# Performance work log

Measured on AMD Instinct MI355X. Metric: run time of the kernel, lower is better.

Reference implementation:

```python
import jax, jax.numpy as jnp
import numpy as np

C = 256      # in_channels
NH = 4       # n_heads
NG = 32      # GroupNorm num_groups
EPS = 1e-5   # torch GroupNorm default eps


def _conv1x1(x, w, b):
    # 1x1 conv == per-pixel channel matmul. x: (B,C,H,W), w: (O,C), b: (O,)
    return jnp.einsum('oc,bchw->bohw', w, x) + b[None, :, None, None]


def _groupnorm(x, gamma, beta):
    b, c, h, w = x.shape
    xg = x.reshape(b, NG, c // NG, h, w)
    mu = xg.mean(axis=(2, 3, 4), keepdims=True)
    var = xg.var(axis=(2, 3, 4), keepdims=True)
    xn = ((xg - mu) * jax.lax.rsqrt(var + EPS)).reshape(b, c, h, w)
    return xn * gamma[None, :, None, None] + beta[None, :, None, None]


def setup_inputs() -> dict:
    key = jax.random.key(0)
    ks = jax.random.split(key, 5)
    B, H, W = 2, 64, 64
    s = 1.0 / np.sqrt(C).astype(np.float32)
    return {
        'x': jax.random.normal(ks[0], (B, C, H, W), jnp.float32),
        'gamma': jnp.ones((C,), jnp.float32),
        'beta': jnp.zeros((C,), jnp.float32),
        'wq': jax.random.normal(ks[1], (C, C), jnp.float32) * s,
        'bq': jnp.zeros((C,), jnp.float32),
        'wk': jax.random.normal(ks[2], (C, C), jnp.float32) * s,
        'bk': jnp.zeros((C,), jnp.float32),
        'wv': jax.random.normal(ks[3], (C, C), jnp.float32) * s,
        'bv': jnp.zeros((C,), jnp.float32),
        'wp': jax.random.normal(ks[4], (C, C), jnp.float32) * s,
        'bp': jnp.zeros((C,), jnp.float32),
    }


def reference(x, gamma, beta, wq, bq, wk, bk, wv, bv, wp, bp):
    b, c, h, w = x.shape
    c_ = c // NH  # head dim
    hn = _groupnorm(x, gamma, beta)
    # NOTE: original splits channels as (head_dim, n_heads) with head_dim leading
    q = _conv1x1(hn, wq, bq).reshape(b, c_, NH, h * w)
    k = _conv1x1(hn, wk, bk).reshape(b, c_, NH, h * w)
    v = _conv1x1(hn, wv, bv).reshape(b, c_, NH, h * w)
    scores = jnp.einsum('bcnq,bcnk->bqkn', q, k) * (c_ ** -0.5)  # (B,S,S,NH)
    attn = jax.nn.softmax(scores, axis=2)  # softmax over key axis
    out = jnp.einsum('bcnd,bqdn->bcnq', v, attn).reshape(b, c, h, w)
    return x + _conv1x1(out, wp, bp)
```

## Files before the change

kernel.cpp:

```cpp
#include <hip/hip_runtime.h>

#define CH 256
#define NHEAD 4
#define HD 64
#define SP 4096
#define NB 2
#define QSCALE 0.1803368801111204f

typedef __attribute__((ext_vector_type(8))) short bf16x8;
typedef __attribute__((ext_vector_type(4))) float f32x4;
typedef unsigned int u32;
typedef unsigned short u16;

__device__ inline u16 b16(float f) {
    u32 u = __float_as_uint(f);
    return (u16)((u + 0x8000u) >> 16);
}
__device__ inline u32 bpack(float lo, float hi) {
    u32 ul = __float_as_uint(lo), uh = __float_as_uint(hi);
    return ((uh + 0x8000u) & 0xffff0000u) | ((ul + 0x8000u) >> 16);
}
__device__ inline float fexp2(float x) { return __builtin_amdgcn_exp2f(x); }

__global__ __launch_bounds__(256) void prep_kernel(
    const float* __restrict__ x, float2* __restrict__ part,
    const float* __restrict__ wq, const float* __restrict__ wk,
    const float* __restrict__ wv, const float* __restrict__ wp,
    u16* __restrict__ wqb, u16* __restrict__ wkb,
    u16* __restrict__ wvb, u16* __restrict__ wpb)
{
    int tid = threadIdx.x;
    if (blockIdx.x < 256) {
        int bgq = blockIdx.x;
        int bg = bgq >> 2, qtr = bgq & 3;
        const float4* xp = (const float4*)(x + (size_t)bg * 8 * SP) + qtr * 2048;
        float s = 0.f, ss = 0.f;
        for (int i = tid; i < 2048; i += 256) {
            float4 u = xp[i];
            s  += (u.x + u.y) + (u.z + u.w);
            ss += (u.x * u.x + u.y * u.y) + (u.z * u.z + u.w * u.w);
        }
#pragma unroll
        for (int off = 32; off > 0; off >>= 1) {
            s  += __shfl_down(s, off);
            ss += __shfl_down(ss, off);
        }
        __shared__ float ws_s[4], ws_q[4];
        int w = tid >> 6;
        if ((tid & 63) == 0) { ws_s[w] = s; ws_q[w] = ss; }
        __syncthreads();
        if (tid == 0)
            part[bgq] = make_float2(ws_s[0] + ws_s[1] + ws_s[2] + ws_s[3],
                                    ws_q[0] + ws_q[1] + ws_q[2] + ws_q[3]);
    } else {
        int idx = (blockIdx.x - 256) * 256 + tid;
        int m = idx >> 16, i = idx & 65535;
        if (m == 0)      wqb[i] = b16(wq[i] * QSCALE);
        else if (m == 1) wkb[i] = b16(wk[i]);
        else if (m == 2) wvb[i] = b16(wv[i]);
        else {
            int c = i >> 8, col = i & 255;
            int n = col & 3, d = col >> 2;
            wpb[c * 256 + n * 64 + d] = b16(wp[i]);
        }
    }
}

__global__ __launch_bounds__(256) void qkv_gemm_kernel(
    const float* __restrict__ x, const float2* __restrict__ part,
    const float* __restrict__ gamma, const float* __restrict__ beta,
    const u16* __restrict__ wqb, const u16* __restrict__ wkb,
    const u16* __restrict__ wvb,
    const float* __restrict__ bq, const float* __restrict__ bk,
    const float* __restrict__ bv,
    u16* __restrict__ qt, u16* __restrict__ ktp, u16* __restrict__ vtp)
{
    int zz = blockIdx.y;
    int b = zz / 3, p = zz % 3;
    const u16* W = (p == 0) ? wqb : (p == 1) ? wkb : wvb;
    const float* bias = (p == 0) ? bq : (p == 1) ? bk : bv;
    float bs = (p == 0) ? QSCALE : 1.f;
    int s0 = blockIdx.x * 32;
    int tid = threadIdx.x, w = tid >> 6, lane = tid & 63;
    int t = lane >> 4, ln = lane & 15;

    __shared__ u16 SB[10240];
    __shared__ float As[256], Bs[256];

    {
        int c = tid, bg = b * 32 + (c >> 3);
        float s = 0.f, ss = 0.f;
#pragma unroll
        for (int q = 0; q < 4; q++) { float2 pp = part[bg * 4 + q]; s += pp.x; ss += pp.y; }
        float mu = s * (1.f / 32768.f);
        float var = ss * (1.f / 32768.f) - mu * mu;
        float rs = rsqrtf(var + 1e-5f);
        float ga = gamma[c];
        As[c] = rs * ga;
        Bs[c] = beta[c] - mu * rs * ga;
    }
    __syncthreads();

    {
        int c2 = (tid >> 3) * 2;
        int sseg = (tid & 7) * 4;
#pragma unroll
        for (int it = 0; it < 4; it++) {
            int c = it * 64 + c2;
            float4 v0 = *(const float4*)&x[((size_t)b * CH + c) * SP + s0 + sseg];
            float4 v1 = *(const float4*)&x[((size_t)b * CH + c + 1) * SP + s0 + sseg];
            float a0 = As[c], b0 = Bs[c], a1 = As[c + 1], b1 = Bs[c + 1];
            float e0[4] = {fmaf(a0, v0.x, b0), fmaf(a0, v0.y, b0),
                           fmaf(a0, v0.z, b0), fmaf(a0, v0.w, b0)};
            float e1[4] = {fmaf(a1, v1.x, b1), fmaf(a1, v1.y, b1),
                           fmaf(a1, v1.z, b1), fmaf(a1, v1.w, b1)};
#pragma unroll
            for (int j = 0; j < 4; j++)
                *(u32*)&SB[(sseg + j) * 264 + c] = bpack(e0[j], e1[j]);
        }
    }
    __syncthreads();

    f32x4 acc[4][2];
#pragma unroll
    for (int og = 0; og < 4; og++)
#pragma unroll
        for (int sg = 0; sg < 2; sg++)
            acc[og][sg] = (f32x4){0.f, 0.f, 0.f, 0.f};

#pragma unroll
    for (int ks = 0; ks < 8; ks++) {
        bf16x8 af[4], bfv[2];
#pragma unroll
        for (int og = 0; og < 4; og++)
            af[og] = *(const bf16x8*)&W[(size_t)(w * 64 + og * 16 + ln) * CH + ks * 32 + t * 8];
#pragma unroll
        for (int sg = 0; sg < 2; sg++)
            bfv[sg] = *(const bf16x8*)&SB[(sg * 16 + ln) * 264 + ks * 32 + t * 8];
#pragma unroll
        for (int og = 0; og < 4; og++)
#pragma unroll
            for (int sg = 0; sg < 2; sg++)
                acc[og][sg] = __builtin_amdgcn_mfma_f32_16x16x32_bf16(
                    af[og], bfv[sg], acc[og][sg], 0, 0, 0);
    }
    __syncthreads();

    if (p < 2) {
#pragma unroll
        for (int og = 0; og < 4; og++)
#pragma unroll
            for (int sg = 0; sg < 2; sg++)
#pragma unroll
                for (int r = 0; r < 4; r++) {
                    int o = w * 64 + og * 16 + 4 * t + r;
                    SB[(r * 32 + sg * 16 + ln) * 72 + (w * 16 + og * 4 + t)] =
                        b16(acc[og][sg][r] + bias[o] * bs);
                }
        __syncthreads();
        if (p == 0) {
#pragma unroll
            for (int it = 0; it < 4; it++) {
                int f = it * 256 + tid;
                int o8 = f & 7, sl = (f >> 3) & 31, n = f >> 8;
                *(uint4*)&qt[((size_t)(b * 4 + n) * SP + s0 + sl) * HD + o8 * 8] =
                    *(const uint4*)&SB[(n * 32 + sl) * 72 + o8 * 8];
            }
        } else {
#pragma unroll
            for (int it = 0; it < 4; it++) {
                int f = it * 256 + tid;
                int o8 = f & 7, sl = (f >> 3) & 31, n = f >> 8;
                int key = s0 + sl;
                int g = ((key >> 4) & 3) * 2 + (o8 >> 2);
                int lp = (key & 15) + 16 * (o8 & 3);
                *(uint4*)&ktp[(size_t)(b * 4 + n) * SP * HD +
                              (size_t)(key >> 6) * 4096 + g * 512 + lp * 8] =
                    *(const uint4*)&SB[(n * 32 + sl) * 72 + o8 * 8];
            }
        }
    } else {
#pragma unroll
        for (int og = 0; og < 4; og++)
#pragma unroll
            for (int sg = 0; sg < 2; sg++)
#pragma unroll
                for (int r = 0; r < 4; r++) {
                    int o = w * 64 + og * 16 + 4 * t + r;
                    SB[(r * 64 + w * 16 + og * 4 + t) * 40 + sg * 16 + ln] =
                        b16(acc[og][sg][r] + bias[o]);
                }
        __syncthreads();
#pragma unroll
        for (int it = 0; it < 4; it++) {
            int f = it * 256 + tid;
            int so8 = f & 3, d = (f >> 2) & 63, n = f >> 8;
            int key = s0 + so8 * 8;
            int g = ((d >> 4) & 3) * 2 + ((key >> 5) & 1);
            int lp = (d & 15) + 16 * ((key >> 3) & 3);
            *(uint4*)&vtp[(size_t)(b * 4 + n) * SP * HD +
                          (size_t)(key >> 6) * 4096 + g * 512 + lp * 8] =
                *(const uint4*)&SB[(n * 64 + d) * 40 + so8 * 8];
        }
    }
}

template <int NT>
__global__ __launch_bounds__(256, 3) void attn_kernel(
    const u16* __restrict__ qtb, const u16* __restrict__ ktp,
    const u16* __restrict__ vtp, u16* __restrict__ opart,
    float* __restrict__ lpart)
{
    int bx = blockIdx.x;
    int z = bx & 7, qt_i = (bx >> 3) & 31, sp = bx >> 8;
    int sq0 = qt_i * 128;
    int tile0 = sp * NT;
    const u16* qz = qtb + (size_t)z * SP * HD;
    const u16* kz = ktp + (size_t)z * SP * HD;
    const u16* vz = vtp + (size_t)z * SP * HD;

    int tid = threadIdx.x, w = tid >> 6, l = tid & 63;
    int t = l >> 4, ln = l & 15;

    __shared__ __align__(16) u32 Pb[4][2][512];

    bf16x8 qf[2][2];
#pragma unroll
    for (int qg = 0; qg < 2; qg++)
#pragma unroll
        for (int ds = 0; ds < 2; ds++)
            qf[qg][ds] = *(const bf16x8*)&qz[
                (size_t)(sq0 + w * 32 + qg * 16 + ln) * HD + ds * 32 + t * 8];

    bf16x8 kf[8], vf[8];
#pragma unroll
    for (int g = 0; g < 8; g++)
        kf[g] = *(const bf16x8*)&kz[(size_t)tile0 * 4096 + g * 512 + l * 8];

    float lsum[2] = {0.f, 0.f};
    f32x4 oacc[2][4];
#pragma unroll
    for (int qg = 0; qg < 2; qg++)
#pragma unroll
        for (int dg = 0; dg < 4; dg++)
            oacc[qg][dg] = (f32x4){0.f, 0.f, 0.f, 0.f};

    const f32x4 z4 = {0.f, 0.f, 0.f, 0.f};
    f32x4 sa[2][4];

    auto ep = [&](int qg) {
#pragma unroll
        for (int kg = 0; kg < 4; kg++) {
            float e0 = fexp2(sa[qg][kg][0]);
            float e1 = fexp2(sa[qg][kg][1]);
            float e2 = fexp2(sa[qg][kg][2]);
            float e3 = fexp2(sa[qg][kg][3]);
            lsum[qg] += (e0 + e1) + (e2 + e3);
            u32 p0 = __builtin_amdgcn_perm(__float_as_uint(e1), __float_as_uint(e0), 0x07060302u);
            u32 p1 = __builtin_amdgcn_perm(__float_as_uint(e3), __float_as_uint(e2), 0x07060302u);
            int Lt = ln + 16 * (2 * (kg & 1) + (t >> 1));
            int ksg = kg >> 1;
            *(uint2*)&Pb[w][qg][(ksg * 64 + Lt) * 4 + 2 * (t & 1)] =
                make_uint2(p0, p1);
        }
    };

#pragma unroll
    for (int kti = 0; kti < NT; kti++) {
        size_t tb = (size_t)(tile0 + kti) * 4096;

#pragma unroll
        for (int g = 0; g < 8; g++)
            vf[g] = *(const bf16x8*)&vz[tb + g * 512 + l * 8];

#pragma unroll
        for (int kg = 0; kg < 4; kg++)
#pragma unroll
            for (int qg = 0; qg < 2; qg++)
                sa[qg][kg] = __builtin_amdgcn_mfma_f32_16x16x32_bf16(
                    kf[kg * 2 + 0], qf[qg][0], z4, 0, 0, 0);
#pragma unroll
        for (int kg = 0; kg < 4; kg++)
#pragma unroll
            for (int qg = 0; qg < 2; qg++)
                sa[qg][kg] = __builtin_amdgcn_mfma_f32_16x16x32_bf16(
                    kf[kg * 2 + 1], qf[qg][1], sa[qg][kg], 0, 0, 0);

        if (kti < NT - 1) {
            size_t nb = tb + 4096;
#pragma unroll
            for (int g = 0; g < 8; g++)
                kf[g] = *(const bf16x8*)&kz[nb + g * 512 + l * 8];
        }

        ep(0);
#pragma unroll
        for (int qg = 0; qg < 2; qg++) {
            if (qg == 0) ep(1);
            bf16x8 pf[2];
#pragma unroll
            for (int ksg = 0; ksg < 2; ksg++)
                pf[ksg] = *(const bf16x8*)&Pb[w][qg][(ksg * 64 + l) * 4];
#pragma unroll
            for (int ksg = 0; ksg < 2; ksg++)
#pragma unroll
                for (int dg = 0; dg < 4; dg++)
                    oacc[qg][dg] = __builtin_amdgcn_mfma_f32_16x16x32_bf16(
                        pf[ksg], vf[dg * 2 + ksg], oacc[qg][dg], 0, 0, 0);
        }
    }

#pragma unroll
    for (int qg = 0; qg < 2; qg++) {
        lsum[qg] += __shfl_xor(lsum[qg], 16);
        lsum[qg] += __shfl_xor(lsum[qg], 32);
    }

    size_t obase = (size_t)(sp * 8 + z) * SP;
    u16* po = (u16*)&Pb[w][0][0];
#pragma unroll
    for (int qg = 0; qg < 2; qg++)
#pragma unroll
        for (int dg = 0; dg < 4; dg++)
#pragma unroll
            for (int r = 0; r < 4; r++)
                po[(qg * 16 + 4 * t + r) * 64 + dg * 16 + ln] = b16(oacc[qg][dg][r]);
#pragma unroll
    for (int i = 0; i < 4; i++) {
        int f = i * 512 + l * 8;
        int qloc = f >> 6, d0 = f & 63;
        uint4 v = *(const uint4*)&po[f];
        *(uint4*)&opart[(obase + sq0 + w * 32 + qloc) * HD + d0] = v;
    }
    if (t == 0)
#pragma unroll
        for (int qg = 0; qg < 2; qg++)
            lpart[obase + sq0 + w * 32 + qg * 16 + ln] = lsum[qg];
}

template <int NSPLIT>
__global__ __launch_bounds__(256) void proj_gemm_kernel(
    const u16* __restrict__ opart, const float* __restrict__ lpart,
    const u16* __restrict__ wpb, const float* __restrict__ bp,
    const float* __restrict__ x, float* __restrict__ out)
{
    int b = blockIdx.y;
    int s0 = blockIdx.x * 16;
    int tid = threadIdx.x, w = tid >> 6, lane = tid & 63;
    int t = lane >> 4, ln = lane & 15;

    __shared__ u16 BsL[16 * 264];

#pragma unroll
    for (int it = 0; it < 2; it++) {
        int f = it * 256 + tid;
        int oct = f & 31, s = f >> 5;
        int n = oct >> 3, d0 = (oct & 7) * 8;
        float lsumv = 0.f;
        float accv[8] = {0.f,0.f,0.f,0.f,0.f,0.f,0.f,0.f};
#pragma unroll
        for (int sp = 0; sp < NSPLIT; sp++) {
            size_t base = (size_t)(sp * 8 + b * 4 + n) * SP + s0 + s;
            lsumv += lpart[base];
            uint4 o4 = *(const uint4*)&opart[base * HD + d0];
            u32 ov[4] = {o4.x, o4.y, o4.z, o4.w};
#pragma unroll
            for (int i = 0; i < 4; i++) {
                accv[2 * i + 0] += __uint_as_float(ov[i] << 16);
                accv[2 * i + 1] += __uint_as_float(ov[i] & 0xffff0000u);
            }
        }
        float inv = 1.f / lsumv;
        u32 res[4];
#pragma unroll
        for (int i = 0; i < 4; i++)
            res[i] = (bpack(accv[2 * i + 0] * inv, accv[2 * i + 1] * inv));
        *(uint4*)&BsL[s * 264 + oct * 8] = make_uint4(res[0], res[1], res[2], res[3]);
    }
    __syncthreads();

    f32x4 acc[4];
#pragma unroll
    for (int og = 0; og < 4; og++)
        acc[og] = (f32x4){0.f, 0.f, 0.f, 0.f};

#pragma unroll
    for (int ks = 0; ks < 8; ks++) {
        bf16x8 af[4];
#pragma unroll
        for (int og = 0; og < 4; og++)
            af[og] = *(const bf16x8*)&wpb[(size_t)(w * 64 + og * 16 + ln) * CH + ks * 32 + t * 8];
        bf16x8 bfv = *(const bf16x8*)&BsL[ln * 264 + ks * 32 + t * 8];
#pragma unroll
        for (int og = 0; og < 4; og++)
            acc[og] = __builtin_amdgcn_mfma_f32_16x16x32_bf16(
                af[og], bfv, acc[og], 0, 0, 0);
    }

#pragma unroll
    for (int og = 0; og < 4; og++)
#pragma unroll
        for (int r = 0; r < 4; r++) {
            int c = w * 64 + og * 16 + 4 * t + r;
            size_t idx = ((size_t)b * CH + c) * SP + s0 + ln;
            out[idx] = acc[og][r] + bp[c] + x[idx];
        }
}

extern "C" void kernel_launch(void* const* d_in, const int* in_sizes, int n_in,
                              void* d_out, int out_size, void* d_ws, size_t ws_size,
                              hipStream_t stream)
{
    const float* x     = (const float*)d_in[0];
    const float* gamma = (const float*)d_in[1];
    const float* beta  = (const float*)d_in[2];
    const float* wq = (const float*)d_in[3]; const float* bq = (const float*)d_in[4];
    const float* wk = (const float*)d_in[5]; const float* bk = (const float*)d_in[6];
    const float* wv = (const float*)d_in[7]; const float* bv = (const float*)d_in[8];
    const float* wp = (const float*)d_in[9]; const float* bp = (const float*)d_in[10];
    float* out = (float*)d_out;

    const size_t TEN = (size_t)8 * SP * HD;
    const size_t NEED8 = 4096 + 524288 + 3 * TEN * 2 + 8 * TEN * 2 + 8 * 8 * SP * 4;
    int nsplit = (ws_size >= NEED8) ? 8 : 4;

    char* wsb = (char*)d_ws;
    float2* part = (float2*)wsb;
    u16* wqb = (u16*)(wsb + 4096);
    u16* wkb = wqb + 65536;
    u16* wvb = wkb + 65536;
    u16* wpb = wvb + 65536;
    u16* qt  = wpb + 65536;
    u16* ktp = qt + TEN;
    u16* vtp = ktp + TEN;
    u16* opart = vtp + TEN;
    float* lpart = (float*)(opart + (size_t)nsplit * TEN);

    prep_kernel<<<dim3(1280), dim3(256), 0, stream>>>(
        x, part, wq, wk, wv, wp, wqb, wkb, wvb, wpb);
    qkv_gemm_kernel<<<dim3(128, 6), dim3(256), 0, stream>>>(
        x, part, gamma, beta, wqb, wkb, wvb, bq, bk, bv, qt, ktp, vtp);
    if (nsplit == 8) {
        attn_kernel<8><<<dim3(2048), dim3(256), 0, stream>>>(
            qt, ktp, vtp, opart, lpart);
        proj_gemm_kernel<8><<<dim3(256, 2), dim3(256), 0, stream>>>(
            opart, lpart, wpb, bp, x, out);
    } else {
        attn_kernel<16><<<dim3(1024), dim3(256), 0, stream>>>(
            qt, ktp, vtp, opart, lpart);
        proj_gemm_kernel<4><<<dim3(256, 2), dim3(256), 0, stream>>>(
            opart, lpart, wpb, bp, x, out);
    }
}
```

Before: 155.0 us.

## Fuse four kernels into one persistent cooperative kernel with grid syncs

Merges the prep, QKV GEMM, attention and projection kernels into one persistent cooperative kernel. Blocks loop over work units for each phase, and grid.sync separates the phases. The aim is to remove the launch overhead and tail gaps between kernels. In exchange it caps occupancy through launch bounds and the occupancy query, adds grid-wide barrier costs, and may lose the higher parallelism of the attention launch.

```diff
diff --git a/kernel.cpp b/kernel.cpp
--- a/kernel.cpp
+++ b/kernel.cpp
@@ -1,10 +1,12 @@
 #include <hip/hip_runtime.h>
+#include <hip/hip_cooperative_groups.h>
+
+namespace cg = cooperative_groups;
 
 #define CH 256
 #define NHEAD 4
 #define HD 64
 #define SP 4096
-#define NB 2
 #define QSCALE 0.1803368801111204f
 
 typedef __attribute__((ext_vector_type(8))) short bf16x8;
@@ -22,389 +24,398 @@
 }
 __device__ inline float fexp2(float x) { return __builtin_amdgcn_exp2f(x); }
 
-__global__ __launch_bounds__(256) void prep_kernel(
+template <int NT>
+__global__ __launch_bounds__(256, 3) void fused_kernel(
     const float* __restrict__ x, float2* __restrict__ part,
+    const float* __restrict__ gamma, const float* __restrict__ beta,
     const float* __restrict__ wq, const float* __restrict__ wk,
     const float* __restrict__ wv, const float* __restrict__ wp,
+    const float* __restrict__ bq, const float* __restrict__ bk,
+    const float* __restrict__ bv, const float* __restrict__ bp,
     u16* __restrict__ wqb, u16* __restrict__ wkb,
-    u16* __restrict__ wvb, u16* __restrict__ wpb)
+    u16* __restrict__ wvb, u16* __restrict__ wpb,
+    u16* __restrict__ qt, u16* __restrict__ ktp, u16* __restrict__ vtp,
+    u16* __restrict__ opart, float* __restrict__ lpart,
+    float* __restrict__ out)
 {
+    constexpr int NSPLIT = 64 / NT;
+    cg::grid_group grid = cg::this_grid();
+    __shared__ __align__(16) char smem[22784];
+
     int tid = threadIdx.x;
-    if (blockIdx.x < 256) {
-        int bgq = blockIdx.x;
-        int bg = bgq >> 2, qtr = bgq & 3;
-        const float4* xp = (const float4*)(x + (size_t)bg * 8 * SP) + qtr * 2048;
-        float s = 0.f, ss = 0.f;
-        for (int i = tid; i < 2048; i += 256) {
-            float4 u = xp[i];
-            s  += (u.x + u.y) + (u.z + u.w);
-            ss += (u.x * u.x + u.y * u.y) + (u.z * u.z + u.w * u.w);
-        }
-#pragma unroll
-        for (int off = 32; off > 0; off >>= 1) {
-            s  += __shfl_down(s, off);
-            ss += __shfl_down(ss, off);
-        }
-        __shared__ float ws_s[4], ws_q[4];
-        int w = tid >> 6;
-        if ((tid & 63) == 0) { ws_s[w] = s; ws_q[w] = ss; }
-        __syncthreads();
-        if (tid == 0)
-            part[bgq] = make_float2(ws_s[0] + ws_s[1] + ws_s[2] + ws_s[3],
-                                    ws_q[0] + ws_q[1] + ws_q[2] + ws_q[3]);
-    } else {
-        int idx = (blockIdx.x - 256) * 256 + tid;
-        int m = idx >> 16, i = idx & 65535;
-        if (m == 0)      wqb[i] = b16(wq[i] * QSCALE);
-        else if (m == 1) wkb[i] = b16(wk[i]);
-        else if (m == 2) wvb[i] = b16(wv[i]);
-        else {
-            int c = i >> 8, col = i & 255;
-            int n = col & 3, d = col >> 2;
-            wpb[c * 256 + n * 64 + d] = b16(wp[i]);
+    int nb = gridDim.x, bid = blockIdx.x;
+    int w = tid >> 6, lane = tid & 63;
+    int t = lane >> 4, ln = lane & 15;
+
+    for (int u = bid; u < 1280; u += nb) {
+        if (u < 256) {
+            int bg = u >> 2, qtr = u & 3;
+            const float4* xp = (const float4*)(x + (size_t)bg * 8 * SP) + qtr * 2048;
+            float s = 0.f, ss = 0.f;
+            for (int i = tid; i < 2048; i += 256) {
+                float4 v = xp[i];
+                s  += (v.x + v.y) + (v.z + v.w);
+                ss += (v.x * v.x + v.y * v.y) + (v.z * v.z + v.w * v.w);
+            }
+#pragma unroll
+            for (int off = 32; off > 0; off >>= 1) {
+                s  += __shfl_down(s, off);
+                ss += __shfl_down(ss, off);
+            }
+            float* ws_s = (float*)smem;
+            float* ws_q = (float*)smem + 4;
+            __syncthreads();
+            if (lane == 0) { ws_s[w] = s; ws_q[w] = ss; }
+            __syncthreads();
+            if (tid == 0)
+                part[u] = make_float2(ws_s[0] + ws_s[1] + ws_s[2] + ws_s[3],
+                                      ws_q[0] + ws_q[1] + ws_q[2] + ws_q[3]);
+        } else {
+            int idx = (u - 256) * 256 + tid;
+            int m = idx >> 16, i = idx & 65535;
+            if (m == 0)      wqb[i] = b16(wq[i] * QSCALE);
+            else if (m == 1) wkb[i] = b16(wk[i]);
+            else if (m == 2) wvb[i] = b16(wv[i]);
+            else {
+                int c = i >> 8, col = i & 255;
+                int n = col & 3, d = col >> 2;
+                wpb[c * 256 + n * 64 + d] = b16(wp[i]);
+            }
         }
     }
-}
-
-__global__ __launch_bounds__(256) void qkv_gemm_kernel(
-    const float* __restrict__ x, const float2* __restrict__ part,
-    const float* __restrict__ gamma, const float* __restrict__ beta,
-    const u16* __restrict__ wqb, const u16* __restrict__ wkb,
-    const u16* __restrict__ wvb,
-    const float* __restrict__ bq, const float* __restrict__ bk,
-    const float* __restrict__ bv,
-    u16* __restrict__ qt, u16* __restrict__ ktp, u16* __restrict__ vtp)
-{
-    int zz = blockIdx.y;
-    int b = zz / 3, p = zz % 3;
-    const u16* W = (p == 0) ? wqb : (p == 1) ? wkb : wvb;
-    const float* bias = (p == 0) ? bq : (p == 1) ? bk : bv;
-    float bs = (p == 0) ? QSCALE : 1.f;
-    int s0 = blockIdx.x * 32;
-    int tid = threadIdx.x, w = tid >> 6, lane = tid & 63;
-    int t = lane >> 4, ln = lane & 15;
-
-    __shared__ u16 SB[10240];
-    __shared__ float As[256], Bs[256];
+    __threadfence();
+    grid.sync();
 
     {
-        int c = tid, bg = b * 32 + (c >> 3);
-        float s = 0.f, ss = 0.f;
-#pragma unroll
-        for (int q = 0; q < 4; q++) { float2 pp = part[bg * 4 + q]; s += pp.x; ss += pp.y; }
-        float mu = s * (1.f / 32768.f);
-        float var = ss * (1.f / 32768.f) - mu * mu;
-        float rs = rsqrtf(var + 1e-5f);
-        float ga = gamma[c];
-        As[c] = rs * ga;
-        Bs[c] = beta[c] - mu * rs * ga;
-    }
-    __syncthreads();
-
-    {
-        int c2 = (tid >> 3) * 2;
-        int sseg = (tid & 7) * 4;
-#pragma unroll
-        for (int it = 0; it < 4; it++) {
-            int c = it * 64 + c2;
-            float4 v0 = *(const float4*)&x[((size_t)b * CH + c) * SP + s0 + sseg];
-            float4 v1 = *(const float4*)&x[((size_t)b * CH + c + 1) * SP + s0 + sseg];
-            float a0 = As[c], b0 = Bs[c], a1 = As[c + 1], b1 = Bs[c + 1];
-            float e0[4] = {fmaf(a0, v0.x, b0), fmaf(a0, v0.y, b0),
-                           fmaf(a0, v0.z, b0), fmaf(a0, v0.w, b0)};
-            float e1[4] = {fmaf(a1, v1.x, b1), fmaf(a1, v1.y, b1),
-                           fmaf(a1, v1.z, b1), fmaf(a1, v1.w, b1)};
-#pragma unroll
-            for (int j = 0; j < 4; j++)
-                *(u32*)&SB[(sseg + j) * 264 + c] = bpack(e0[j], e1[j]);
+        float* As = (float*)smem;
+        float* Bs = (float*)(smem + 1024);
+        u16*   SB = (u16*)(smem + 2048);
+
+        for (int u = bid; u < 768; u += nb) {
+            int zz = u / 128;
+            int b = zz / 3, p = zz % 3;
+            const u16* W = (p == 0) ? wqb : (p == 1) ? wkb : wvb;
+            const float* bias = (p == 0) ? bq : (p == 1) ? bk : bv;
+            float bs = (p == 0) ? QSCALE : 1.f;
+            int s0 = (u % 128) * 32;
+
+            __syncthreads();
+
+            {
+                int c = tid, bg = b * 32 + (c >> 3);
+                float s = 0.f, ss = 0.f;
+#pragma unroll
+                for (int q = 0; q < 4; q++) {
+                    float2 pp = part[bg * 4 + q]; s += pp.x; ss += pp.y;
+                }
+                float mu = s * (1.f / 32768.f);
+                float var = ss * (1.f / 32768.f) - mu * mu;
+                float rs = rsqrtf(var + 1e-5f);
+                float ga = gamma[c];
+                As[c] = rs * ga;
+                Bs[c] = beta[c] - mu * rs * ga;
+            }
+            __syncthreads();
+
+            {
+                int c2 = (tid >> 3) * 2, sseg = (tid & 7) * 4;
+#pragma unroll
+                for (int it = 0; it < 4; it++) {
+                    int c = it * 64 + c2;
+                    float4 v0 = *(const float4*)&x[((size_t)b * CH + c) * SP + s0 + sseg];
+                    float4 v1 = *(const float4*)&x[((size_t)b * CH + c + 1) * SP + s0 + sseg];
+                    float a0 = As[c], b0 = Bs[c], a1 = As[c + 1], b1 = Bs[c + 1];
+                    float e0[4] = {fmaf(a0, v0.x, b0), fmaf(a0, v0.y, b0),
+                                   fmaf(a0, v0.z, b0), fmaf(a0, v0.w, b0)};
+                    float e1[4] = {fmaf(a1, v1.x, b1), fmaf(a1, v1.y, b1),
+                                   fmaf(a1, v1.z, b1), fmaf(a1, v1.w, b1)};
+#pragma unroll
+                    for (int j = 0; j < 4; j++)
+                        *(u32*)&SB[(sseg + j) * 264 + c] = bpack(e0[j], e1[j]);
+                }
+            }
+            __syncthreads();
+
+            f32x4 acc[4][2];
+#pragma unroll
+            for (int og = 0; og < 4; og++)
+#pragma unroll
+                for (int sg = 0; sg < 2; sg++)
+                    acc[og][sg] = (f32x4){0.f, 0.f, 0.f, 0.f};
+
+#pragma unroll
+            for (int ks = 0; ks < 8; ks++) {
+                bf16x8 af[4], bfv[2];
+#pragma unroll
+                for (int og = 0; og < 4; og++)
+                    af[og] = *(const bf16x8*)&W[(size_t)(w * 64 + og * 16 + ln) * CH + ks * 32 + t * 8];
+#pragma unroll
+                for (int sg = 0; sg < 2; sg++)
+                    bfv[sg] = *(const bf16x8*)&SB[(sg * 16 + ln) * 264 + ks * 32 + t * 8];
+#pragma unroll
+                for (int og = 0; og < 4; og++)
+#pragma unroll
+                    for (int sg = 0; sg < 2; sg++)
+                        acc[og][sg] = __builtin_amdgcn_mfma_f32_16x16x32_bf16(
+                            af[og], bfv[sg], acc[og][sg], 0, 0, 0);
+            }
+            __syncthreads();
+
+            if (p < 2) {
+#pragma unroll
+                for (int og = 0; og < 4; og++)
+#pragma unroll
+                    for (int sg = 0; sg < 2; sg++)
+#pragma unroll
+                        for (int r = 0; r < 4; r++) {
+                            int o = w * 64 + og * 16 + 4 * t + r;
+                            SB[(r * 32 + sg * 16 + ln) * 72 + (w * 16 + og * 4 + t)] =
+                                b16(acc[og][sg][r] + bias[o] * bs);
+                        }
+                __syncthreads();
+                if (p == 0) {
+#pragma unroll
+                    for (int it = 0; it < 4; it++) {
+                        int f = it * 256 + tid;
+                        int o8 = f & 7, sl = (f >> 3) & 31, n = f >> 8;
+                        *(uint4*)&qt[((size_t)(b * 4 + n) * SP + s0 + sl) * HD + o8 * 8] =
+                            *(const uint4*)&SB[(n * 32 + sl) * 72 + o8 * 8];
+                    }
+                } else {
+#pragma unroll
+                    for (int it = 0; it < 4; it++) {
+                        int f = it * 256 + tid;
+                        int o8 = f & 7, sl = (f >> 3) & 31, n = f >> 8;
+                        int key = s0 + sl;
+                        int g = ((key >> 4) & 3) * 2 + (o8 >> 2);
+                        int lp = (key & 15) + 16 * (o8 & 3);
+                        *(uint4*)&ktp[(size_t)(b * 4 + n) * SP * HD +
+                                      (size_t)(key >> 6) * 4096 + g * 512 + lp * 8] =
+                            *(const uint4*)&SB[(n * 32 + sl) * 72 + o8 * 8];
+                    }
+                }
+            } else {
+#pragma unroll
+                for (int og = 0; og < 4; og++)
+#pragma unroll
+                    for (int sg = 0; sg < 2; sg++)
+#pragma unroll
+                        for (int r = 0; r < 4; r++) {
+                            int o = w * 64 + og * 16 + 4 * t + r;
+                            SB[(r * 64 + w * 16 + og * 4 + t) * 40 + sg * 16 + ln] =
+                                b16(acc[og][sg][r] + bias[o]);
+                        }
+                __syncthreads();
+#pragma unroll
+                for (int it = 0; it < 4; it++) {
+                    int f = it * 256 + tid;
+                    int so8 = f & 3, d = (f >> 2) & 63, n = f >> 8;
+                    int key = s0 + so8 * 8;
+                    int g = ((d >> 4) & 3) * 2 + ((key >> 5) & 1);
+                    int lp = (d & 15) + 16 * ((key >> 3) & 3);
+                    *(uint4*)&vtp[(size_t)(b * 4 + n) * SP * HD +
+                                  (size_t)(key >> 6) * 4096 + g * 512 + lp * 8] =
+                        *(const uint4*)&SB[(n * 64 + d) * 40 + so8 * 8];
+                }
+            }
         }
     }
-    __syncthreads();
-
-    f32x4 acc[4][2];
-#pragma unroll
-    for (int og = 0; og < 4; og++)
-#pragma unroll
-        for (int sg = 0; sg < 2; sg++)
-            acc[og][sg] = (f32x4){0.f, 0.f, 0.f, 0.f};
-
-#pragma unroll
-    for (int ks = 0; ks < 8; ks++) {
-        bf16x8 af[4], bfv[2];
-#pragma unroll
-        for (int og = 0; og < 4; og++)
-            af[og] = *(const bf16x8*)&W[(size_t)(w * 64 + og * 16 + ln) * CH + ks * 32 + t * 8];
-#pragma unroll
-        for (int sg = 0; sg < 2; sg++)
-            bfv[sg] = *(const bf16x8*)&SB[(sg * 16 + ln) * 264 + ks * 32 + t * 8];
-#pragma unroll
-        for (int og = 0; og < 4; og++)
-#pragma unroll
-            for (int sg = 0; sg < 2; sg++)
-                acc[og][sg] = __builtin_amdgcn_mfma_f32_16x16x32_bf16(
-                    af[og], bfv[sg], acc[og][sg], 0, 0, 0);
-    }
-    __syncthreads();
-
-    if (p < 2) {
-#pragma unroll
-        for (int og = 0; og < 4; og++)
-#pragma unroll
-            for (int sg = 0; sg < 2; sg++)
-#pragma unroll
-                for (int r = 0; r < 4; r++) {
-                    int o = w * 64 + og * 16 + 4 * t + r;
-                    SB[(r * 32 + sg * 16 + ln) * 72 + (w * 16 + og * 4 + t)] =
-                        b16(acc[og][sg][r] + bias[o] * bs);
-                }
-        __syncthreads();
-        if (p == 0) {
-#pragma unroll
-            for (int it = 0; it < 4; it++) {
-                int f = it * 256 + tid;
-                int o8 = f & 7, sl = (f >> 3) & 31, n = f >> 8;
-                *(uint4*)&qt[((size_t)(b * 4 + n) * SP + s0 + sl) * HD + o8 * 8] =
-                    *(const uint4*)&SB[(n * 32 + sl) * 72 + o8 * 8];
-            }
-        } else {
-#pragma unroll
-            for (int it = 0; it < 4; it++) {
-                int f = it * 256 + tid;
-                int o8 = f & 7, sl = (f >> 3) & 31, n = f >> 8;
-                int key = s0 + sl;
-                int g = ((key >> 4) & 3) * 2 + (o8 >> 2);
-                int lp = (key & 15) + 16 * (o8 & 3);
-                *(uint4*)&ktp[(size_t)(b * 4 + n) * SP * HD +
-                              (size_t)(key >> 6) * 4096 + g * 512 + lp * 8] =
-                    *(const uint4*)&SB[(n * 32 + sl) * 72 + o8 * 8];
-            }
-        }
-    } else {
-#pragma unroll
-        for (int og = 0; og < 4; og++)
-#pragma unroll
-            for (int sg = 0; sg < 2; sg++)
-#pragma unroll
-                for (int r = 0; r < 4; r++) {
-                    int o = w * 64 + og * 16 + 4 * t + r;
-                    SB[(r * 64 + w * 16 + og * 4 + t) * 40 + sg * 16 + ln] =
-                        b16(acc[og][sg][r] + bias[o]);
-                }
-        __syncthreads();
-#pragma unroll
-        for (int it = 0; it < 4; it++) {
-            int f = it * 256 + tid;
-            int so8 = f & 3, d = (f >> 2) & 63, n = f >> 8;
-            int key = s0 + so8 * 8;
-            int g = ((d >> 4) & 3) * 2 + ((key >> 5) & 1);
-            int lp = (d & 15) + 16 * ((key >> 3) & 3);
-            *(uint4*)&vtp[(size_t)(b * 4 + n) * SP * HD +
-                          (size_t)(key >> 6) * 4096 + g * 512 + lp * 8] =
-                *(const uint4*)&SB[(n * 64 + d) * 40 + so8 * 8];
+    __threadfence();
+    grid.sync();
+
+    {
+        u32* Pbw = (u32*)smem + w * 1024;
+
+        for (int u = bid; u < 256 * NSPLIT; u += nb) {
+            int z = u & 7, qt_i = (u >> 3) & 31, sp = u >> 8;
+            int sq0 = qt_i * 128;
+            int tile0 = sp * NT;
+            const u16* qz = qt  + (size_t)z * SP * HD;
+            const u16* kz = ktp + (size_t)z * SP * HD;
+            const u16* vz = vtp + (size_t)z * SP * HD;
+
+            bf16x8 qf[2][2];
+#pragma unroll
+            for (int qg = 0; qg < 2; qg++)
+#pragma unroll
+                for (int ds = 0; ds < 2; ds++)
+                    qf[qg][ds] = *(const bf16x8*)&qz[
+                        (size_t)(sq0 + w * 32 + qg * 16 + ln) * HD + ds * 32 + t * 8];
+
+            bf16x8 kf[8], vf[8];
+#pragma unroll
+            for (int g = 0; g < 8; g++)
+                kf[g] = *(const bf16x8*)&kz[(size_t)tile0 * 4096 + g * 512 + lane * 8];
+
+            float lsum[2] = {0.f, 0.f};
+            f32x4 oacc[2][4];
+#pragma unroll
+            for (int qg = 0; qg < 2; qg++)
+#pragma unroll
+                for (int dg = 0; dg < 4; dg++)
+                    oacc[qg][dg] = (f32x4){0.f, 0.f, 0.f, 0.f};
+
+            const f32x4 z4 = {0.f, 0.f, 0.f, 0.f};
+            f32x4 sa[2][4];
+
+            auto ep = [&](int qg) {
+#pragma unroll
+                for (int kg = 0; kg < 4; kg++) {
+                    float e0 = fexp2(sa[qg][kg][0]);
+                    float e1 = fexp2(sa[qg][kg][1]);
+                    float e2 = fexp2(sa[qg][kg][2]);
+                    float e3 = fexp2(sa[qg][kg][3]);
+                    lsum[qg] += (e0 + e1) + (e2 + e3);
+                    u32 p0 = __builtin_amdgcn_perm(__float_as_uint(e1), __float_as_uint(e0), 0x07060302u);
+                    u32 p1 = __builtin_amdgcn_perm(__float_as_uint(e3), __float_as_uint(e2), 0x07060302u);
+                    int Lt = ln + 16 * (2 * (kg & 1) + (t >> 1));
+                    int ksg = kg >> 1;
+                    *(uint2*)&Pbw[qg * 512 + (ksg * 64 + Lt) * 4 + 2 * (t & 1)] =
+                        make_uint2(p0, p1);
+                }
+            };
+
+#pragma unroll
+            for (int kti = 0; kti < NT; kti++) {
+                size_t tb = (size_t)(tile0 + kti) * 4096;
+
+#pragma unroll
+                for (int g = 0; g < 8; g++)
+                    vf[g] = *(const bf16x8*)&vz[tb + g * 512 + lane * 8];
+
+#pragma unroll
+                for (int kg = 0; kg < 4; kg++)
+#pragma unroll
+                    for (int qg = 0; qg < 2; qg++)
+                        sa[qg][kg] = __builtin_amdgcn_mfma_f32_16x16x32_bf16(
+                            kf[kg * 2 + 0], qf[qg][0], z4, 0, 0, 0);
+#pragma unroll
+                for (int kg = 0; kg < 4; kg++)
+#pragma unroll
+                    for (int qg = 0; qg < 2; qg++)
+                        sa[qg][kg] = __builtin_amdgcn_mfma_f32_16x16x32_bf16(
+                            kf[kg * 2 + 1], qf[qg][1], sa[qg][kg], 0, 0, 0);
+
+                if (kti < NT - 1) {
+                    size_t nbase = tb + 4096;
+#pragma unroll
+                    for (int g = 0; g < 8; g++)
+                        kf[g] = *(const bf16x8*)&kz[nbase + g * 512 + lane * 8];
+                }
+
+                ep(0);
+#pragma unroll
+                for (int qg = 0; qg < 2; qg++) {
+                    if (qg == 0) ep(1);
+                    bf16x8 pf[2];
+#pragma unroll
+                    for (int ksg = 0; ksg < 2; ksg++)
+                        pf[ksg] = *(const bf16x8*)&Pbw[qg * 512 + (ksg * 64 + lane) * 4];
+#pragma unroll
+                    for (int ksg = 0; ksg < 2; ksg++)
+#pragma unroll
+                        for (int dg = 0; dg < 4; dg++)
+                            oacc[qg][dg] = __builtin_amdgcn_mfma_f32_16x16x32_bf16(
+                                pf[ksg], vf[dg * 2 + ksg], oacc[qg][dg], 0, 0, 0);
+                }
+            }
+
+#pragma unroll
+            for (int qg = 0; qg < 2; qg++) {
+                lsum[qg] += __shfl_xor(lsum[qg], 16);
+                lsum[qg] += __shfl_xor(lsum[qg], 32);
+            }
+
+            size_t obase = (size_t)(sp * 8 + z) * SP;
+            u16* po = (u16*)Pbw;
+#pragma unroll
+            for (int qg = 0; qg < 2; qg++)
+#pragma unroll
+                for (int dg = 0; dg < 4; dg++)
+#pragma unroll
+                    for (int r = 0; r < 4; r++)
+                        po[(qg * 16 + 4 * t + r) * 64 + dg * 16 + ln] = b16(oacc[qg][dg][r]);
+#pragma unroll
+            for (int i = 0; i < 4; i++) {
+                int f = i * 512 + lane * 8;
+                int qloc = f >> 6, d0 = f & 63;
+                uint4 v = *(const uint4*)&po[f];
+                *(uint4*)&opart[(obase + sq0 + w * 32 + qloc) * HD + d0] = v;
+            }
+            if (t == 0)
+#pragma unroll
+                for (int qg = 0; qg < 2; qg++)
+                    lpart[obase + sq0 + w * 32 + qg * 16 + ln] = lsum[qg];
         }
     }
-}
-
-template <int NT>
-__global__ __launch_bounds__(256, 3) void attn_kernel(
-    const u16* __restrict__ qtb, const u16* __restrict__ ktp,
-    const u16* __restrict__ vtp, u16* __restrict__ opart,
-    float* __restrict__ lpart)
-{
-    int bx = blockIdx.x;
-    int z = bx & 7, qt_i = (bx >> 3) & 31, sp = bx >> 8;
-    int sq0 = qt_i * 128;
-    int tile0 = sp * NT;
-    const u16* qz = qtb + (size_t)z * SP * HD;
-    const u16* kz = ktp + (size_t)z * SP * HD;
-    const u16* vz = vtp + (size_t)z * SP * HD;
-
-    int tid = threadIdx.x, w = tid >> 6, l = tid & 63;
-    int t = l >> 4, ln = l & 15;
-
-    __shared__ __align__(16) u32 Pb[4][2][512];
-
-    bf16x8 qf[2][2];
-#pragma unroll
-    for (int qg = 0; qg < 2; qg++)
-#pragma unroll
-        for (int ds = 0; ds < 2; ds++)
-            qf[qg][ds] = *(const bf16x8*)&qz[
-                (size_t)(sq0 + w * 32 + qg * 16 + ln) * HD + ds * 32 + t * 8];
-
-    bf16x8 kf[8], vf[8];
-#pragma unroll
-    for (int g = 0; g < 8; g++)
-        kf[g] = *(const bf16x8*)&kz[(size_t)tile0 * 4096 + g * 512 + l * 8];
-
-    float lsum[2] = {0.f, 0.f};
-    f32x4 oacc[2][4];
-#pragma unroll
-    for (int qg = 0; qg < 2; qg++)
-#pragma unroll
-        for (int dg = 0; dg < 4; dg++)
-            oacc[qg][dg] = (f32x4){0.f, 0.f, 0.f, 0.f};
-
-    const f32x4 z4 = {0.f, 0.f, 0.f, 0.f};
-    f32x4 sa[2][4];
-
-    auto ep = [&](int qg) {
-#pragma unroll
-        for (int kg = 0; kg < 4; kg++) {
-            float e0 = fexp2(sa[qg][kg][0]);
-            float e1 = fexp2(sa[qg][kg][1]);
-            float e2 = fexp2(sa[qg][kg][2]);
-            float e3 = fexp2(sa[qg][kg][3]);
-            lsum[qg] += (e0 + e1) + (e2 + e3);
-            u32 p0 = __builtin_amdgcn_perm(__float_as_uint(e1), __float_as_uint(e0), 0x07060302u);
-            u32 p1 = __builtin_amdgcn_perm(__float_as_uint(e3), __float_as_uint(e2), 0x07060302u);
-            int Lt = ln + 16 * (2 * (kg & 1) + (t >> 1));
-            int ksg = kg >> 1;
-            *(uint2*)&Pb[w][qg][(ksg * 64 + Lt) * 4 + 2 * (t & 1)] =
-                make_uint2(p0, p1);
-        }
-    };
-
-#pragma unroll
-    for (int kti = 0; kti < NT; kti++) {
-        size_t tb = (size_t)(tile0 + kti) * 4096;
-
-#pragma unroll
-        for (int g = 0; g < 8; g++)
-            vf[g] = *(const bf16x8*)&vz[tb + g * 512 + l * 8];
-
-#pragma unroll
-        for (int kg = 0; kg < 4; kg++)
-#pragma unroll
-            for (int qg = 0; qg < 2; qg++)
-                sa[qg][kg] = __builtin_amdgcn_mfma_f32_16x16x32_bf16(
-                    kf[kg * 2 + 0], qf[qg][0], z4, 0, 0, 0);
-#pragma unroll
-        for (int kg = 0; kg < 4; kg++)
-#pragma unroll
-            for (int qg = 0; qg < 2; qg++)
-                sa[qg][kg] = __builtin_amdgcn_mfma_f32_16x16x32_bf16(
-                    kf[kg * 2 + 1], qf[qg][1], sa[qg][kg], 0, 0, 0);
-
-        if (kti < NT - 1) {
-            size_t nb = tb + 4096;
-#pragma unroll
-            for (int g = 0; g < 8; g++)
-                kf[g] = *(const bf16x8*)&kz[nb + g * 512 + l * 8];
-        }
-
-        ep(0);
-#pragma unroll
-        for (int qg = 0; qg < 2; qg++) {
-            if (qg == 0) ep(1);
-            bf16x8 pf[2];
-#pragma unroll
-            for (int ksg = 0; ksg < 2; ksg++)
-                pf[ksg] = *(const bf16x8*)&Pb[w][qg][(ksg * 64 + l) * 4];
-#pragma unroll
-            for (int ksg = 0; ksg < 2; ksg++)
-#pragma unroll
-                for (int dg = 0; dg < 4; dg++)
-                    oacc[qg][dg] = __builtin_amdgcn_mfma_f32_16x16x32_bf16(
-                        pf[ksg], vf[dg * 2 + ksg], oacc[qg][dg], 0, 0, 0);
+    __threadfence();
+    grid.sync();
+
+    {
+        u16* BsL = (u16*)smem;
+
+        for (int u = bid; u < 512; u += nb) {
+            int b = u >> 8;
+            int s0 = (u & 255) * 16;
+
+            __syncthreads();
+
+#pragma unroll
+            for (int it = 0; it < 2; it++) {
+                int f = it * 256 + tid;
+                int oct = f & 31, s = f >> 5;
+                int n = oct >> 3, d0 = (oct & 7) * 8;
+                float lsumv = 0.f;
+                float accv[8] = {0.f,0.f,0.f,0.f,0.f,0.f,0.f,0.f};
+#pragma unroll
+                for (int sp = 0; sp < NSPLIT; sp++) {
+                    size_t base = (size_t)(sp * 8 + b * 4 + n) * SP + s0 + s;
+                    lsumv += lpart[base];
+                    uint4 o4 = *(const uint4*)&opart[base * HD + d0];
+                    u32 ov[4] = {o4.x, o4.y, o4.z, o4.w};
+#pragma unroll
+                    for (int i = 0; i < 4; i++) {
+                        accv[2 * i + 0] += __uint_as_float(ov[i] << 16);
+                        accv[2 * i + 1] += __uint_as_float(ov[i] & 0xffff0000u);
+                    }
+                }
+                float inv = 1.f / lsumv;
+                u32 res[4];
+#pragma unroll
+                for (int i = 0; i < 4; i++)
+                    res[i] = bpack(accv[2 * i + 0] * inv, accv[2 * i + 1] * inv);
+                *(uint4*)&BsL[s * 264 + oct * 8] = make_uint4(res[0], res[1], res[2], res[3]);
+            }
+            __syncthreads();
+
+            f32x4 acc[4];
+#pragma unroll
+            for (int og = 0; og < 4; og++)
+                acc[og] = (f32x4){0.f, 0.f, 0.f, 0.f};
+
+#pragma unroll
+            for (int ks = 0; ks < 8; ks++) {
+                bf16x8 af[4];
+#pragma unroll
+                for (int og = 0; og < 4; og++)
+                    af[og] = *(const bf16x8*)&wpb[(size_t)(w * 64 + og * 16 + ln) * CH + ks * 32 + t * 8];
+                bf16x8 bfv = *(const bf16x8*)&BsL[ln * 264 + ks * 32 + t * 8];
+#pragma unroll
+                for (int og = 0; og < 4; og++)
+                    acc[og] = __builtin_amdgcn_mfma_f32_16x16x32_bf16(
+                        af[og], bfv, acc[og], 0, 0, 0);
+            }
+
+#pragma unroll
+            for (int og = 0; og < 4; og++)
+#pragma unroll
+                for (int r = 0; r < 4; r++) {
+                    int c = w * 64 + og * 16 + 4 * t + r;
+                    size_t idx = ((size_t)b * CH + c) * SP + s0 + ln;
+                    out[idx] = acc[og][r] + bp[c] + x[idx];
+                }
         }
     }
-
-#pragma unroll
-    for (int qg = 0; qg < 2; qg++) {
-        lsum[qg] += __shfl_xor(lsum[qg], 16);
-        lsum[qg] += __shfl_xor(lsum[qg], 32);
-    }
-
-    size_t obase = (size_t)(sp * 8 + z) * SP;
-    u16* po = (u16*)&Pb[w][0][0];
-#pragma unroll
-    for (int qg = 0; qg < 2; qg++)
-#pragma unroll
-        for (int dg = 0; dg < 4; dg++)
-#pragma unroll
-            for (int r = 0; r < 4; r++)
-                po[(qg * 16 + 4 * t + r) * 64 + dg * 16 + ln] = b16(oacc[qg][dg][r]);
-#pragma unroll
-    for (int i = 0; i < 4; i++) {
-        int f = i * 512 + l * 8;
-        int qloc = f >> 6, d0 = f & 63;
-        uint4 v = *(const uint4*)&po[f];
-        *(uint4*)&opart[(obase + sq0 + w * 32 + qloc) * HD + d0] = v;
-    }
-    if (t == 0)
-#pragma unroll
-        for (int qg = 0; qg < 2; qg++)
-            lpart[obase + sq0 + w * 32 + qg * 16 + ln] = lsum[qg];
-}
-
-template <int NSPLIT>
-__global__ __launch_bounds__(256) void proj_gemm_kernel(
-    const u16* __restrict__ opart, const float* __restrict__ lpart,
-    const u16* __restrict__ wpb, const float* __restrict__ bp,
-    const float* __restrict__ x, float* __restrict__ out)
-{
-    int b = blockIdx.y;
-    int s0 = blockIdx.x * 16;
-    int tid = threadIdx.x, w = tid >> 6, lane = tid & 63;
-    int t = lane >> 4, ln = lane & 15;
-
-    __shared__ u16 BsL[16 * 264];
-
-#pragma unroll
-    for (int it = 0; it < 2; it++) {
-        int f = it * 256 + tid;
-        int oct = f & 31, s = f >> 5;
-        int n = oct >> 3, d0 = (oct & 7) * 8;
-        float lsumv = 0.f;
-        float accv[8] = {0.f,0.f,0.f,0.f,0.f,0.f,0.f,0.f};
-#pragma unroll
-        for (int sp = 0; sp < NSPLIT; sp++) {
-            size_t base = (size_t)(sp * 8 + b * 4 + n) * SP + s0 + s;
-            lsumv += lpart[base];
-            uint4 o4 = *(const uint4*)&opart[base * HD + d0];
-            u32 ov[4] = {o4.x, o4.y, o4.z, o4.w};
-#pragma unroll
-            for (int i = 0; i < 4; i++) {
-                accv[2 * i + 0] += __uint_as_float(ov[i] << 16);
-                accv[2 * i + 1] += __uint_as_float(ov[i] & 0xffff0000u);
-            }
-        }
-        float inv = 1.f / lsumv;
-        u32 res[4];
-#pragma unroll
-        for (int i = 0; i < 4; i++)
-            res[i] = (bpack(accv[2 * i + 0] * inv, accv[2 * i + 1] * inv));
-        *(uint4*)&BsL[s * 264 + oct * 8] = make_uint4(res[0], res[1], res[2], res[3]);
-    }
-    __syncthreads();
-
-    f32x4 acc[4];
-#pragma unroll
-    for (int og = 0; og < 4; og++)
-        acc[og] = (f32x4){0.f, 0.f, 0.f, 0.f};
-
-#pragma unroll
-    for (int ks = 0; ks < 8; ks++) {
-        bf16x8 af[4];
-#pragma unroll
-        for (int og = 0; og < 4; og++)
-            af[og] = *(const bf16x8*)&wpb[(size_t)(w * 64 + og * 16 + ln) * CH + ks * 32 + t * 8];
-        bf16x8 bfv = *(const bf16x8*)&BsL[ln * 264 + ks * 32 + t * 8];
-#pragma unroll
-        for (int og = 0; og < 4; og++)
-            acc[og] = __builtin_amdgcn_mfma_f32_16x16x32_bf16(
-                af[og], bfv, acc[og], 0, 0, 0);
-    }
-
-#pragma unroll
-    for (int og = 0; og < 4; og++)
-#pragma unroll
-        for (int r = 0; r < 4; r++) {
-            int c = w * 64 + og * 16 + 4 * t + r;
-            size_t idx = ((size_t)b * CH + c) * SP + s0 + ln;
-            out[idx] = acc[og][r] + bp[c] + x[idx];
-        }
 }
 
 extern "C" void kernel_launch(void* const* d_in, const int* in_sizes, int n_in,
@@ -436,19 +447,33 @@
     u16* opart = vtp + TEN;
     float* lpart = (float*)(opart + (size_t)nsplit * TEN);
 
-    prep_kernel<<<dim3(1280), dim3(256), 0, stream>>>(
-        x, part, wq, wk, wv, wp, wqb, wkb, wvb, wpb);
-    qkv_gemm_kernel<<<dim3(128, 6), dim3(256), 0, stream>>>(
-        x, part, gamma, beta, wqb, wkb, wvb, bq, bk, bv, qt, ktp, vtp);
-    if (nsplit == 8) {
-        attn_kernel<8><<<dim3(2048), dim3(256), 0, stream>>>(
-            qt, ktp, vtp, opart, lpart);
-        proj_gemm_kernel<8><<<dim3(256, 2), dim3(256), 0, stream>>>(
-            opart, lpart, wpb, bp, x, out);
-    } else {
-        attn_kernel<16><<<dim3(1024), dim3(256), 0, stream>>>(
-            qt, ktp, vtp, opart, lpart);
-        proj_gemm_kernel<4><<<dim3(256, 2), dim3(256), 0, stream>>>(
-            opart, lpart, wpb, bp, x, out);
-    }
+    void* args[] = {
+        (void*)&x, (void*)&part, (void*)&gamma, (void*)&beta,
+        (void*)&wq, (void*)&wk, (void*)&wv, (void*)&wp,
+        (void*)&bq, (void*)&bk, (void*)&bv, (void*)&bp,
+        (void*)&wqb, (void*)&wkb, (void*)&wvb, (void*)&wpb,
+        (void*)&qt, (void*)&ktp, (void*)&vtp,
+        (void*)&opart, (void*)&lpart, (void*)&out
+    };
+
+    int maxb = 0;
+    hipError_t oe;
+    if (nsplit == 8)
+        oe = hipOccupancyMaxActiveBlocksPerMultiprocessor(
+            &maxb, reinterpret_cast<const void*>(fused_kernel<8>), 256, 0);
+    else
+        oe = hipOccupancyMaxActiveBlocksPerMultiprocessor(
+            &maxb, reinterpret_cast<const void*>(fused_kernel<16>), 256, 0);
+    if (oe != hipSuccess || maxb < 1) maxb = 2;
+    if (maxb > 8) maxb = 8;
+    int gridsz = maxb * 256;
+
+    if (nsplit == 8)
+        hipLaunchCooperativeKernel(
+            reinterpret_cast<const void*>(fused_kernel<8>),
+            dim3(gridsz), dim3(256), args, 0, stream);
+    else
+        hipLaunchCooperativeKernel(
+            reinterpret_cast<const void*>(fused_kernel<16>),
+            dim3(gridsz), dim3(256), args, 0, stream);
 }
```

After: 375.3 us. 2.42x slower.
